# Kernel optimization log

Measured on AMD Instinct MI355X. Metric: run time of the kernel, lower is better.

## Reference

```python
import jax, jax.numpy as jnp
import numpy as np

Q_MAX = 127.0  # 2^(8-1) - 1 for 8-bit activations


def _ste_round(x):
    # forward: round(x); backward: identity
    return x + jax.lax.stop_gradient(jnp.round(x) - x)


def setup_inputs() -> dict:
    key = jax.random.key(0)
    k1, k2 = jax.random.split(key)
    B, S, D_IN, D_OUT = 4, 4096, 2048, 2048
    x = jax.random.normal(k1, (B, S, D_IN), dtype=jnp.float32)
    # muP-style init: std = 1/sqrt(fan_in)
    weight = jax.random.normal(k2, (D_OUT, D_IN), dtype=jnp.float32) / np.sqrt(D_IN)
    return {"x": x, "weight": weight}


def reference(x, weight):
    # --- ternary weight quantization (AbsMean) ---
    w_scale = jnp.maximum(jnp.mean(jnp.abs(weight)), 1e-6)        # scalar
    w_norm = weight / w_scale
    w_quant = jnp.clip(_ste_round(w_norm), -1.0, 1.0)             # [O, I], values in {-1,0,1}

    # --- per-token absmax activation quantization (8-bit) ---
    a_scale = jnp.clip(jnp.max(jnp.abs(x), axis=-1, keepdims=True), 1e-8, None)  # [B,S,1]
    x_quant = jnp.clip(_ste_round(x * (Q_MAX / a_scale)), -Q_MAX, Q_MAX)         # [B,S,I]

    # --- scaled matmul: y = (x_q @ w_q^T) * w_scale * (a_scale / Q_MAX) ---
    y = jnp.einsum('bsi,oi->bso', x_quant, w_quant)
    y = y * (w_scale * (a_scale / Q_MAX))
    return y
```

## Files before the change

### kernel.cpp

```cpp
#include <hip/hip_runtime.h>
#include <hip/hip_bf16.h>

typedef int int4v __attribute__((ext_vector_type(4)));

#define K_DIM 2048
#define N_DIM 2048
#define M_DIM 16384
#define NW 4194304
#define BKB 128
#define NKT (K_DIM / BKB)

__global__ void k_wsum(const float4* __restrict__ w4, double* __restrict__ red) {
  const int n4 = NW / 4;
  double s = 0.0;
  for (int i = blockIdx.x * blockDim.x + threadIdx.x; i < n4; i += gridDim.x * blockDim.x) {
    float4 v = w4[i];
    s += (double)fabsf(v.x) + (double)fabsf(v.y) + (double)fabsf(v.z) + (double)fabsf(v.w);
  }
  for (int o = 32; o; o >>= 1) s += __shfl_xor(s, o);
  __shared__ double sd[4];
  if ((threadIdx.x & 63) == 0) sd[threadIdx.x >> 6] = s;
  __syncthreads();
  if (threadIdx.x == 0) red[blockIdx.x] = (sd[0] + sd[1]) + (sd[2] + sd[3]);
}

__global__ void k_wscale(const double* __restrict__ red, double* __restrict__ wsd) {
  double s = red[threadIdx.x];
  for (int o = 32; o; o >>= 1) s += __shfl_xor(s, o);
  __shared__ double sd[4];
  if ((threadIdx.x & 63) == 0) sd[threadIdx.x >> 6] = s;
  __syncthreads();
  if (threadIdx.x == 0) {
    double m = ((sd[0] + sd[1]) + (sd[2] + sd[3])) / (double)NW;
    *wsd = (m > 1e-6) ? m : 1e-6;
  }
}

__device__ __forceinline__ char wq1(float v, double ws) {
  double r = rint((double)v / ws);
  r = fmin(fmax(r, -1.0), 1.0);
  return (char)(int)r;
}

__global__ void k_wquant(const float4* __restrict__ w4, const double* __restrict__ wsd,
                         char4* __restrict__ wq4) {
  int i = blockIdx.x * blockDim.x + threadIdx.x;
  if (i >= NW / 4) return;
  double ws = *wsd;
  float4 v = w4[i];
  char4 q;
  q.x = wq1(v.x, ws);
  q.y = wq1(v.y, ws);
  q.z = wq1(v.z, ws);
  q.w = wq1(v.w, ws);
  wq4[i] = q;
}

__device__ __forceinline__ char qi8(float v, double rr) {
  double q = rint((double)v * rr);
  q = fmin(fmax(q, -127.0), 127.0);
  return (char)(int)q;
}

__global__ void k_xquant(const float* __restrict__ x, float* __restrict__ ascale,
                         char* __restrict__ xq) {
  const int row = blockIdx.x;
  const int t = threadIdx.x;
  const float4* xr = (const float4*)(x + (size_t)row * K_DIM);
  float4 v0 = xr[t];
  float4 v1 = xr[t + 256];
  float m = fmaxf(fmaxf(fmaxf(fabsf(v0.x), fabsf(v0.y)), fmaxf(fabsf(v0.z), fabsf(v0.w))),
                  fmaxf(fmaxf(fabsf(v1.x), fabsf(v1.y)), fmaxf(fabsf(v1.z), fabsf(v1.w))));
  for (int o = 32; o; o >>= 1) m = fmaxf(m, __shfl_xor(m, o));
  __shared__ float sm[4];
  if ((t & 63) == 0) sm[t >> 6] = m;
  __syncthreads();
  float a = fmaxf(fmaxf(sm[0], sm[1]), fmaxf(sm[2], sm[3]));
  a = fmaxf(a, 1e-8f);
  if (t == 0) ascale[row] = a;
  double rr = 127.0 / (double)a;
  char4* qr4 = (char4*)(xq + (size_t)row * K_DIM);
  char4 a4, b4;
  a4.x = qi8(v0.x, rr); a4.y = qi8(v0.y, rr); a4.z = qi8(v0.z, rr); a4.w = qi8(v0.w, rr);
  b4.x = qi8(v1.x, rr); b4.y = qi8(v1.y, rr); b4.z = qi8(v1.z, rr); b4.w = qi8(v1.w, rr);
  qr4[t] = a4;
  qr4[t + 256] = b4;
}

__device__ __forceinline__ void gload16(const void* g, void* l) {
  __builtin_amdgcn_global_load_lds(
      (const __attribute__((address_space(1))) void*)g,
      (__attribute__((address_space(3))) void*)l, 16, 0, 0);
}

#define RD_A(DST, CA, MH, CO)                                               \
  _Pragma("unroll") for (int mf = 0; mf < 4; ++mf)                          \
    DST[mf] = *(const int4v*)((CA) + (rA + (MH)*64 + mf * 16) * 128 + (CO));

#define RD_B(DST, CB, CO)                                                   \
  _Pragma("unroll") for (int nf = 0; nf < 4; ++nf)                          \
    DST[nf] = *(const int4v*)((CB) + (rB + nf * 16) * 128 + (CO));

#define MM(MH, AF, BF)                                                      \
  __builtin_amdgcn_s_setprio(1);                                            \
  _Pragma("unroll") for (int mf = 0; mf < 4; ++mf)                          \
  _Pragma("unroll") for (int nf = 0; nf < 4; ++nf)                          \
    acc[(MH)*4 + mf][nf] = __builtin_amdgcn_mfma_i32_16x16x64_i8(           \
        AF[mf], BF[nf], acc[(MH)*4 + mf][nf], 0, 0, 0);                     \
  __builtin_amdgcn_s_setprio(0);

#define CFENCE asm volatile("" ::: "memory")
#define BAR    do { CFENCE; __builtin_amdgcn_s_barrier(); CFENCE; } while (0)

#define TILE(CA, CB, NA, NB, KT)                                            \
  {                                                                         \
    const char* An = Ab + (((KT) + 1) & (NKT - 1)) * BKB;                   \
    const char* Bn = Bb + (((KT) + 1) & (NKT - 1)) * BKB;                   \
        \
    RD_A(afY, CA, 1, co0);                                                  \
    _Pragma("unroll") for (int c = 0; c < 4; ++c)                           \
      gload16(An + soff[c], (NA) + loff[c]);                                \
    BAR;                                                                    \
    MM(0, afX, bfP);                                                        \
    BAR;                                                                    \
       \
    RD_A(afX, CA, 0, co1);                                                  \
    RD_B(bfQ, CB, co1);                                                     \
    _Pragma("unroll") for (int c = 0; c < 4; ++c)                           \
      gload16(Bn + soff[c], (NB) + loff[c]);                                \
    BAR;                                                                    \
    MM(1, afY, bfP);                                                        \
    BAR;                                                                    \
                        \
    RD_A(afY, CA, 1, co1);                                                  \
    BAR;                                                                    \
    MM(0, afX, bfQ);                                                        \
    BAR;                                                                    \
        \
    asm volatile("s_waitcnt vmcnt(0)" ::: "memory");                        \
    BAR;                \
    RD_A(afX, NA, 0, co0);                                                  \
    RD_B(bfP, NB, co0);                                                     \
    MM(1, afY, bfQ);                                                        \
    BAR;                                                                    \
  }

__global__ __launch_bounds__(512, 1) void k_gemm(
    const char* __restrict__ xq, const char* __restrict__ wq,
    const float* __restrict__ ascale, const double* __restrict__ wsd,
    float* __restrict__ out) {
  __shared__ __align__(16) char lds[131072];
  char* lA0 = lds;
  char* lB0 = lds + 32768;
  char* lA1 = lds + 65536;
  char* lB1 = lds + 98304;

  const int tid = threadIdx.x;
  const int l = tid & 63;
  const int wv = tid >> 6;
  const int wm = wv >> 2;
  const int wn = wv & 3;
  const int g = l >> 4, r16 = l & 15;

  const int bid = blockIdx.x;
  const int logical = (bid & 7) * 64 + (bid >> 3);
  const int br = logical >> 3;
  const int bc = logical & 7;

  const char* Ab = xq + (size_t)br * 256 * K_DIM;
  const char* Bb = wq + (size_t)bc * 256 * K_DIM;

  int soff[4], loff[4];
#pragma unroll
  for (int c = 0; c < 4; ++c) {
    int lb = c * 8192 + tid * 16;
    loff[c] = lb;
    int row = lb >> 7;
    int cb = lb & 127;
    soff[c] = row * K_DIM + (cb ^ ((row & 7) << 4));
  }

  const int sw = (r16 & 7) << 4;
  const int co0 = (g * 16) ^ sw;
  const int co1 = (64 + g * 16) ^ sw;
  const int rA = wm * 128 + r16;
  const int rB = wn * 64 + r16;

  int4v acc[8][4];
#pragma unroll
  for (int mf = 0; mf < 8; ++mf)
#pragma unroll
    for (int nf = 0; nf < 4; ++nf) acc[mf][nf] = (int4v){0, 0, 0, 0};

#pragma unroll
  for (int c = 0; c < 4; ++c) gload16(Ab + soff[c], lA0 + loff[c]);
#pragma unroll
  for (int c = 0; c < 4; ++c) gload16(Bb + soff[c], lB0 + loff[c]);
  asm volatile("s_waitcnt vmcnt(0)" ::: "memory");
  BAR;

  int4v afA0[4], afA1[4], bfB0[4], bfB1[4];
#define afX afA0
#define afY afA1
#define bfP bfB0
#define bfQ bfB1

  RD_A(afX, lA0, 0, co0);
  RD_B(bfP, lB0, co0);

  for (int kt = 0; kt < NKT; kt += 2) {
    TILE(lA0, lB0, lA1, lB1, kt);
    TILE(lA1, lB1, lA0, lB0, kt + 1);
  }

  float wsf = (float)(*wsd);
  size_t trow0 = (size_t)br * 256 + wm * 128;
  int oc0 = bc * 256 + wn * 64;
#pragma unroll
  for (int mf = 0; mf < 8; ++mf) {
#pragma unroll
    for (int j = 0; j < 4; ++j) {
      size_t t = trow0 + mf * 16 + g * 4 + j;
      float s = wsf * (ascale[t] / 127.0f);
      float* yr = out + t * (size_t)N_DIM + oc0;
#pragma unroll
      for (int nf = 0; nf < 4; ++nf) yr[nf * 16 + r16] = (float)acc[mf][nf][j] * s;
    }
  }
}

extern "C" void kernel_launch(void* const* d_in, const int* in_sizes, int n_in,
                              void* d_out, int out_size, void* d_ws, size_t ws_size,
                              hipStream_t stream) {
  const float* x = (const float*)d_in[0];
  const float* w = (const float*)d_in[1];
  float* out = (float*)d_out;

  char* ws = (char*)d_ws;
  double* red = (double*)ws;
  double* wsd = (double*)(ws + 2048);
  float* ascale = (float*)(ws + 4096);
  char* xq = (char*)(ws + 4096 + 65536);
  char* wq = xq + (size_t)M_DIM * K_DIM;

  k_wsum<<<256, 256, 0, stream>>>((const float4*)w, red);
  k_wscale<<<1, 256, 0, stream>>>(red, wsd);
  k_wquant<<<NW / 4 / 256, 256, 0, stream>>>((const float4*)w, wsd, (char4*)wq);
  k_xquant<<<M_DIM, 256, 0, stream>>>(x, ascale, xq);
  k_gemm<<<dim3(N_DIM / 256 * M_DIM / 256), 512, 0, stream>>>(xq, wq, ascale, wsd, out);
}
```

Baseline: 127.4 us.

## Restructure GEMM tile pipeline with split global loads and partial vmcnt waits

Reworks the per-tile schedule of the int8 MFMA GEMM. Fragments are now read from LDS right before each MFMA block, using a single A/B fragment set instead of double-buffered register fragments. The global-to-LDS prefetch is spread in pairs across the four phases, with explicit lgkmcnt(0) and vmcnt(2) waits replacing the full vmcnt(0) drain. The aim is to cut register pressure and spread memory traffic more evenly. In exchange, LDS-read latency is no longer hidden behind the previous MFMA block, and the partial vmcnt waits depend on the exact ordering of loads to stay correct.

```diff
diff --git a/kernel.cpp b/kernel.cpp
--- a/kernel.cpp
+++ b/kernel.cpp
@@ -109,40 +109,44 @@
         AF[mf], BF[nf], acc[(MH)*4 + mf][nf], 0, 0, 0);                     \
   __builtin_amdgcn_s_setprio(0);
 
-#define CFENCE asm volatile("" ::: "memory")
-#define BAR    do { CFENCE; __builtin_amdgcn_s_barrier(); CFENCE; } while (0)
+#define SBAR   __builtin_amdgcn_s_barrier()
+#define LGKM0  asm volatile("s_waitcnt lgkmcnt(0)" ::: "memory")
+#define VM2    asm volatile("s_waitcnt vmcnt(2)" ::: "memory")
 
 #define TILE(CA, CB, NA, NB, KT)                                            \
   {                                                                         \
     const char* An = Ab + (((KT) + 1) & (NKT - 1)) * BKB;                   \
     const char* Bn = Bb + (((KT) + 1) & (NKT - 1)) * BKB;                   \
+           \
+    RD_A(af, CA, 0, co0);                                                   \
+    RD_B(bf, CB, co0);                                                      \
+    gload16(An + soff[0], (NA) + loff[0]);                                  \
+    gload16(An + soff[2], (NA) + loff[2]);                                  \
+    SBAR; LGKM0;                                                            \
+    MM(0, af, bf);                                                          \
+    VM2; SBAR;                                                              \
+                           \
+    RD_A(af, CA, 1, co0);                                                   \
+    gload16(Bn + soff[0], (NB) + loff[0]);                                  \
+    gload16(Bn + soff[1], (NB) + loff[1]);                                  \
+    SBAR; LGKM0;                                                            \
+    MM(1, af, bf);                                                          \
+    SBAR;                                                                   \
+                                     \
+    RD_A(af, CA, 0, co1);                                                   \
+    RD_B(bf, CB, co1);                                                      \
+    gload16(Bn + soff[2], (NB) + loff[2]);                                  \
+    gload16(Bn + soff[3], (NB) + loff[3]);                                  \
+    SBAR; LGKM0;                                                            \
+    MM(0, af, bf);                                                          \
+    SBAR;                                                                   \
         \
-    RD_A(afY, CA, 1, co0);                                                  \
-    _Pragma("unroll") for (int c = 0; c < 4; ++c)                           \
-      gload16(An + soff[c], (NA) + loff[c]);                                \
-    BAR;                                                                    \
-    MM(0, afX, bfP);                                                        \
-    BAR;                                                                    \
-       \
-    RD_A(afX, CA, 0, co1);                                                  \
-    RD_B(bfQ, CB, co1);                                                     \
-    _Pragma("unroll") for (int c = 0; c < 4; ++c)                           \
-      gload16(Bn + soff[c], (NB) + loff[c]);                                \
-    BAR;                                                                    \
-    MM(1, afY, bfP);                                                        \
-    BAR;                                                                    \
-                        \
-    RD_A(afY, CA, 1, co1);                                                  \
-    BAR;                                                                    \
-    MM(0, afX, bfQ);                                                        \
-    BAR;                                                                    \
-        \
-    asm volatile("s_waitcnt vmcnt(0)" ::: "memory");                        \
-    BAR;                \
-    RD_A(afX, NA, 0, co0);                                                  \
-    RD_B(bfP, NB, co0);                                                     \
-    MM(1, afY, bfQ);                                                        \
-    BAR;                                                                    \
+    RD_A(af, CA, 1, co1);                                                   \
+    gload16(An + soff[1], (NA) + loff[1]);                                  \
+    gload16(An + soff[3], (NA) + loff[3]);                                  \
+    SBAR; LGKM0;                                                            \
+    MM(1, af, bf);                                                          \
+    VM2; SBAR;                                                              \
   }
 
 __global__ __launch_bounds__(512, 1) void k_gemm(
@@ -197,16 +201,9 @@
 #pragma unroll
   for (int c = 0; c < 4; ++c) gload16(Bb + soff[c], lB0 + loff[c]);
   asm volatile("s_waitcnt vmcnt(0)" ::: "memory");
-  BAR;
-
-  int4v afA0[4], afA1[4], bfB0[4], bfB1[4];
-#define afX afA0
-#define afY afA1
-#define bfP bfB0
-#define bfQ bfB1
-
-  RD_A(afX, lA0, 0, co0);
-  RD_B(bfP, lB0, co0);
+  SBAR;
+
+  int4v af[4], bf[4];
 
   for (int kt = 0; kt < NKT; kt += 2) {
     TILE(lA0, lB0, lA1, lB1, kt);
```

Result: no change. 126.5 us (-0.8%).
